# Kernel optimization log

Measured on AMD Instinct MI355X. Metric: run time of the kernel, lower is better.

## Reference

```python
import jax, jax.numpy as jnp
import numpy as np

B, T, D = 4, 4096, 768      # batch, tokens, n_embd
S = 1024                    # memory_slots (divides T -> adaptive pool == window mean)
K = 8                       # memory_topk
RW = 0.1                    # memory_retrieval_weight


def setup_inputs() -> dict:
    key = jax.random.key(0)
    ks = jax.random.split(key, 10)
    w = 1.0 / np.sqrt(D).astype(np.float32)
    return {
        "x": jax.random.normal(ks[0], (B, T, D), jnp.float32),
        "Wq": jax.random.normal(ks[1], (D, D), jnp.float32) * w,
        "bq": jnp.zeros((D,), jnp.float32),
        "Wk": jax.random.normal(ks[2], (D, D), jnp.float32) * w,
        "bk": jnp.zeros((D,), jnp.float32),
        "Wv": jax.random.normal(ks[3], (D, D), jnp.float32) * w,
        "bv": jnp.zeros((D,), jnp.float32),
        "Wp": jax.random.normal(ks[4], (D, D), jnp.float32) * w,
        "bp": jnp.zeros((D,), jnp.float32),
        "persistent_memory": jax.random.normal(ks[5], (S, D), jnp.float32),
    }


def reference(x, Wq, bq, Wk, bk, Wv, bv, Wp, bp, persistent_memory):
    # _build_memory_slots: adaptive_avg_pool1d to S slots; T % S == 0 so it is a window mean
    pooled = x.reshape(B, S, T // S, D).mean(axis=2)                    # [B,S,D]
    pers = jnp.broadcast_to(persistent_memory[None], (B, S, D))         # persistent bank
    slots = jnp.concatenate([pooled, pers], axis=1)                     # [B,2S,D]

    q = x @ Wq + bq                                                     # [B,T,D]
    k = slots @ Wk + bk                                                 # [B,2S,D]
    v = slots @ Wv + bv                                                 # [B,2S,D]

    scores = jnp.einsum('btd,bsd->bts', q, k) / jnp.sqrt(jnp.float32(D))  # [B,T,2S]
    top_s, top_i = jax.lax.top_k(scores, K)                             # [B,T,K]
    w = jax.nn.softmax(top_s, axis=-1)                                  # softmax over top-k only

    # gather top-k values: [B,T,K,D]
    vg = jnp.take_along_axis(v, top_i.reshape(B, T * K)[:, :, None], axis=1)
    vg = vg.reshape(B, T, K, D)
    retrieved = jnp.einsum('btk,btkd->btd', w, vg)                      # weighted combine

    return RW * (retrieved @ Wp + bp)                                   # proj * retrieval_weight
```

## Files before the change

kernel.cpp:

```cpp
#include <hip/hip_runtime.h>
#include <math.h>

#define BB 4
#define TT 4096
#define DD 768
#define SS 1024
#define S2 2048
#define KTOP 8
#define RWEIGHT 0.1f
#define TAU 2e-4f
#define AMB_CAP 64

typedef __attribute__((ext_vector_type(8))) _Float16 f16x8;
typedef __attribute__((ext_vector_type(4))) float f32x4;
typedef _Float16 f16;

__global__ __launch_bounds__(256) void build_pooled_all(
    const float* __restrict__ x, float* __restrict__ slots)
{
    int i = blockIdx.x * 256 + threadIdx.x;
    int s2 = i / DD;
    int d = i - s2 * DD;
    int b = s2 >> 10, s = s2 & 1023;
    const float* xb = x + (size_t)b * TT * DD + (size_t)(4 * s) * DD + d;
    slots[i] = 0.25f * (xb[0] + xb[DD] + xb[2 * DD] + xb[3 * DD]);
}

__global__ __launch_bounds__(256) void transpose_all(
    const float* __restrict__ W0, const float* __restrict__ W1,
    const float* __restrict__ W2, const float* __restrict__ W3,
    float* __restrict__ T0, float* __restrict__ T1,
    float* __restrict__ T2, float* __restrict__ T3)
{
    const float* W = (blockIdx.z == 0) ? W0 : (blockIdx.z == 1) ? W1
                   : (blockIdx.z == 2) ? W2 : W3;
    float* WT = (blockIdx.z == 0) ? T0 : (blockIdx.z == 1) ? T1
              : (blockIdx.z == 2) ? T2 : T3;
    __shared__ float t[32][33];
    int bx = blockIdx.x * 32, by = blockIdx.y * 32;
    int lx = threadIdx.x & 31, ly = threadIdx.x >> 5;
#pragma unroll
    for (int r = 0; r < 32; r += 8)
        t[ly + r][lx] = W[(size_t)(bx + ly + r) * 768 + by + lx];
    __syncthreads();
#pragma unroll
    for (int r = 0; r < 32; r += 8)
        WT[(size_t)(by + ly + r) * 768 + bx + lx] = t[lx][ly + r];
}

__global__ void zeroN(int* p) { p[threadIdx.x] = 0; }

__global__ __launch_bounds__(256) void producers(
    const float* __restrict__ xq, const float* __restrict__ aslots,
    const f16* __restrict__ aproj,
    const float* __restrict__ WqT, const float* __restrict__ WkT,
    const float* __restrict__ WvT, const float* __restrict__ WpT,
    const float* __restrict__ bq, const float* __restrict__ bk,
    const float* __restrict__ bv, const float* __restrict__ bp,
    f16* __restrict__ qh, f16* __restrict__ qm,
    f16* __restrict__ kh, f16* __restrict__ km,
    f16* __restrict__ v16, float* __restrict__ oproj,
    int n_q, int n_kv, int rowoff)
{
    __shared__ f16 LAh[4096], LAm[4096], LBh[4096], LBm[4096];
    const int tid = threadIdx.x;
    const int lane = tid & 63;
    const int wc = (tid >> 6) & 1;
    const int wr = (tid >> 7) & 1;

    int t = blockIdx.x, mode, bx, by;
    if (t < n_q) { mode = 0; bx = t % 6; by = t / 6; }
    else if (t < n_q + n_kv) { mode = 1; int u = t - n_q; bx = u % 6; by = u / 6; }
    else if (t < n_q + 2 * n_kv) { mode = 2; int u = t - n_q - n_kv; bx = u % 6; by = u / 6; }
    else { mode = 3; int u = t - n_q - 2 * n_kv; bx = u % 6; by = u / 6; }

    const int srow = tid >> 1, c0 = tid & 1;
    const int p0 = c0 ^ (srow & 3) ^ ((srow >> 2) & 1);
    const int wo0 = srow * 32 + p0 * 8, wo1 = wo0 ^ 16;
    const int csw = (((lane >> 4) ^ (lane & 3) ^ ((lane >> 2) & 1)) * 8);
    const int arow0 = by * 128;
    const size_t bn = (size_t)bx * 128;

    f32x4 acc[4][4];
#pragma unroll
    for (int i = 0; i < 4; ++i)
#pragma unroll
        for (int j = 0; j < 4; ++j) acc[i][j] = (f32x4){0.f, 0.f, 0.f, 0.f};

    const int orow0 = wr * 64 + (lane >> 4) * 4;
    const int ocol0 = wc * 64 + (lane & 15);

    if (mode <= 1) {
        const float* A  = (mode == 0) ? xq : aslots;
        const float* BT = (mode == 0) ? WqT : WkT;
        const float* bi = (mode == 0) ? bq : bk;
        f16* Ch = (mode == 0) ? qh : kh;
        f16* Cm = (mode == 0) ? qm : km;
        const int crow0 = ((mode == 0) ? 0 : rowoff) + arow0;
        const float* pa = A + (size_t)(arow0 + srow) * 768 + c0 * 8;
        const float* pb = BT + (bn + srow) * 768 + c0 * 8;

        for (int k0 = 0; k0 < 768; k0 += 32) {
            float4 a0 = *(const float4*)(pa + k0);
            float4 a1 = *(const float4*)(pa + k0 + 4);
            float4 a2 = *(const float4*)(pa + k0 + 16);
            float4 a3 = *(const float4*)(pa + k0 + 20);
            float4 b0 = *(const float4*)(pb + k0);
            float4 b1 = *(const float4*)(pb + k0 + 4);
            float4 b2 = *(const float4*)(pb + k0 + 16);
            float4 b3 = *(const float4*)(pb + k0 + 20);
            __syncthreads();
            {
                float av[16] = {a0.x, a0.y, a0.z, a0.w, a1.x, a1.y, a1.z, a1.w,
                                a2.x, a2.y, a2.z, a2.w, a3.x, a3.y, a3.z, a3.w};
                float bv2[16] = {b0.x, b0.y, b0.z, b0.w, b1.x, b1.y, b1.z, b1.w,
                                 b2.x, b2.y, b2.z, b2.w, b3.x, b3.y, b3.z, b3.w};
                f16x8 h, m;
#pragma unroll
                for (int j = 0; j < 8; ++j) {
                    f16 hh = (f16)av[j]; h[j] = hh; m[j] = (f16)(av[j] - (float)hh);
                }
                *(f16x8*)&LAh[wo0] = h; *(f16x8*)&LAm[wo0] = m;
#pragma unroll
                for (int j = 0; j < 8; ++j) {
                    f16 hh = (f16)av[j + 8]; h[j] = hh; m[j] = (f16)(av[j + 8] - (float)hh);
                }
                *(f16x8*)&LAh[wo1] = h; *(f16x8*)&LAm[wo1] = m;
#pragma unroll
                for (int j = 0; j < 8; ++j) {
                    f16 hh = (f16)bv2[j]; h[j] = hh; m[j] = (f16)(bv2[j] - (float)hh);
                }
                *(f16x8*)&LBh[wo0] = h; *(f16x8*)&LBm[wo0] = m;
#pragma unroll
                for (int j = 0; j < 8; ++j) {
                    f16 hh = (f16)bv2[j + 8]; h[j] = hh; m[j] = (f16)(bv2[j + 8] - (float)hh);
                }
                *(f16x8*)&LBh[wo1] = h; *(f16x8*)&LBm[wo1] = m;
            }
            __syncthreads();

            f16x8 fah[4], fam[4], fbh[4], fbm[4];
#pragma unroll
            for (int mi = 0; mi < 4; ++mi) {
                int off = (wr * 64 + mi * 16 + (lane & 15)) * 32 + csw;
                fah[mi] = *(const f16x8*)&LAh[off];
                fam[mi] = *(const f16x8*)&LAm[off];
            }
#pragma unroll
            for (int ni = 0; ni < 4; ++ni) {
                int off = (wc * 64 + ni * 16 + (lane & 15)) * 32 + csw;
                fbh[ni] = *(const f16x8*)&LBh[off];
                fbm[ni] = *(const f16x8*)&LBm[off];
            }
#pragma unroll
            for (int mi = 0; mi < 4; ++mi)
#pragma unroll
                for (int ni = 0; ni < 4; ++ni) {
                    acc[mi][ni] = __builtin_amdgcn_mfma_f32_16x16x32_f16(
                        fah[mi], fbh[ni], acc[mi][ni], 0, 0, 0);
                    acc[mi][ni] = __builtin_amdgcn_mfma_f32_16x16x32_f16(
                        fah[mi], fbm[ni], acc[mi][ni], 0, 0, 0);
                    acc[mi][ni] = __builtin_amdgcn_mfma_f32_16x16x32_f16(
                        fam[mi], fbh[ni], acc[mi][ni], 0, 0, 0);
                }
        }
#pragma unroll
        for (int mi = 0; mi < 4; ++mi)
#pragma unroll
            for (int ni = 0; ni < 4; ++ni) {
                size_t col = bn + ocol0 + ni * 16;
                float badd = bi[col];
                size_t rbase = (size_t)crow0 + orow0 + mi * 16;
#pragma unroll
                for (int r = 0; r < 4; ++r) {
                    float val = acc[mi][ni][r] + badd;
                    f16 h = (f16)val;
                    size_t idx = (rbase + r) * 768 + col;
                    Ch[idx] = h;
                    Cm[idx] = (f16)(val - (float)h);
                }
            }
    } else if (mode == 2) {
        const int crow0 = rowoff + arow0;
        const float* pa = aslots + (size_t)(arow0 + srow) * 768 + c0 * 8;
        const float* pb = WvT + (bn + srow) * 768 + c0 * 8;
        for (int k0 = 0; k0 < 768; k0 += 32) {
            float4 a0 = *(const float4*)(pa + k0);
            float4 a1 = *(const float4*)(pa + k0 + 4);
            float4 a2 = *(const float4*)(pa + k0 + 16);
            float4 a3 = *(const float4*)(pa + k0 + 20);
            float4 b0 = *(const float4*)(pb + k0);
            float4 b1 = *(const float4*)(pb + k0 + 4);
            float4 b2 = *(const float4*)(pb + k0 + 16);
            float4 b3 = *(const float4*)(pb + k0 + 20);
            __syncthreads();
            {
                f16x8 h;
                h[0] = (f16)a0.x; h[1] = (f16)a0.y; h[2] = (f16)a0.z; h[3] = (f16)a0.w;
                h[4] = (f16)a1.x; h[5] = (f16)a1.y; h[6] = (f16)a1.z; h[7] = (f16)a1.w;
                *(f16x8*)&LAh[wo0] = h;
                h[0] = (f16)a2.x; h[1] = (f16)a2.y; h[2] = (f16)a2.z; h[3] = (f16)a2.w;
                h[4] = (f16)a3.x; h[5] = (f16)a3.y; h[6] = (f16)a3.z; h[7] = (f16)a3.w;
                *(f16x8*)&LAh[wo1] = h;
                h[0] = (f16)b0.x; h[1] = (f16)b0.y; h[2] = (f16)b0.z; h[3] = (f16)b0.w;
                h[4] = (f16)b1.x; h[5] = (f16)b1.y; h[6] = (f16)b1.z; h[7] = (f16)b1.w;
                *(f16x8*)&LBh[wo0] = h;
                h[0] = (f16)b2.x; h[1] = (f16)b2.y; h[2] = (f16)b2.z; h[3] = (f16)b2.w;
                h[4] = (f16)b3.x; h[5] = (f16)b3.y; h[6] = (f16)b3.z; h[7] = (f16)b3.w;
                *(f16x8*)&LBh[wo1] = h;
            }
            __syncthreads();
            f16x8 fah[4], fbh[4];
#pragma unroll
            for (int mi = 0; mi < 4; ++mi)
                fah[mi] = *(const f16x8*)&LAh[(wr * 64 + mi * 16 + (lane & 15)) * 32 + csw];
#pragma unroll
            for (int ni = 0; ni < 4; ++ni)
                fbh[ni] = *(const f16x8*)&LBh[(wc * 64 + ni * 16 + (lane & 15)) * 32 + csw];
#pragma unroll
            for (int mi = 0; mi < 4; ++mi)
#pragma unroll
                for (int ni = 0; ni < 4; ++ni)
                    acc[mi][ni] = __builtin_amdgcn_mfma_f32_16x16x32_f16(
                        fah[mi], fbh[ni], acc[mi][ni], 0, 0, 0);
        }
#pragma unroll
        for (int mi = 0; mi < 4; ++mi)
#pragma unroll
            for (int ni = 0; ni < 4; ++ni) {
                size_t col = bn + ocol0 + ni * 16;
                float badd = bv[col];
                size_t rbase = (size_t)crow0 + orow0 + mi * 16;
#pragma unroll
                for (int r = 0; r < 4; ++r)
                    v16[(rbase + r) * 768 + col] = (f16)(acc[mi][ni][r] + badd);
            }
    } else {
        const f16* pa = aproj + (size_t)(arow0 + srow) * 768 + c0 * 8;
        const float* pb = WpT + (bn + srow) * 768 + c0 * 8;
        for (int k0 = 0; k0 < 768; k0 += 32) {
            f16x8 ah0 = *(const f16x8*)(pa + k0);
            f16x8 ah1 = *(const f16x8*)(pa + k0 + 16);
            float4 b0 = *(const float4*)(pb + k0);
            float4 b1 = *(const float4*)(pb + k0 + 4);
            float4 b2 = *(const float4*)(pb + k0 + 16);
            float4 b3 = *(const float4*)(pb + k0 + 20);
            __syncthreads();
            *(f16x8*)&LAh[wo0] = ah0;
            *(f16x8*)&LAh[wo1] = ah1;
            {
                f16x8 h;
                h[0] = (f16)b0.x; h[1] = (f16)b0.y; h[2] = (f16)b0.z; h[3] = (f16)b0.w;
                h[4] = (f16)b1.x; h[5] = (f16)b1.y; h[6] = (f16)b1.z; h[7] = (f16)b1.w;
                *(f16x8*)&LBh[wo0] = h;
                h[0] = (f16)b2.x; h[1] = (f16)b2.y; h[2] = (f16)b2.z; h[3] = (f16)b2.w;
                h[4] = (f16)b3.x; h[5] = (f16)b3.y; h[6] = (f16)b3.z; h[7] = (f16)b3.w;
                *(f16x8*)&LBh[wo1] = h;
            }
            __syncthreads();
            f16x8 fah[4], fbh[4];
#pragma unroll
            for (int mi = 0; mi < 4; ++mi)
                fah[mi] = *(const f16x8*)&LAh[(wr * 64 + mi * 16 + (lane & 15)) * 32 + csw];
#pragma unroll
            for (int ni = 0; ni < 4; ++ni)
                fbh[ni] = *(const f16x8*)&LBh[(wc * 64 + ni * 16 + (lane & 15)) * 32 + csw];
#pragma unroll
            for (int mi = 0; mi < 4; ++mi)
#pragma unroll
                for (int ni = 0; ni < 4; ++ni)
                    acc[mi][ni] = __builtin_amdgcn_mfma_f32_16x16x32_f16(
                        fah[mi], fbh[ni], acc[mi][ni], 0, 0, 0);
        }
#pragma unroll
        for (int mi = 0; mi < 4; ++mi)
#pragma unroll
            for (int ni = 0; ni < 4; ++ni) {
                size_t col = bn + ocol0 + ni * 16;
                float badd = RWEIGHT * bp[col];
                size_t rbase = (size_t)arow0 + orow0 + mi * 16;
#pragma unroll
                for (int r = 0; r < 4; ++r)
                    oproj[(rbase + r) * 768 + col] = RWEIGHT * acc[mi][ni][r] + badd;
            }
    }
}

__global__ __launch_bounds__(256) void scores_planes(
    const f16* __restrict__ qh, const f16* __restrict__ qm,
    const f16* __restrict__ kh, const f16* __restrict__ km,
    float* __restrict__ C, float alpha)
{
    __shared__ f16 LAh[4096], LAm[4096], LBh[4096], LBm[4096];
    const int tid = threadIdx.x;
    const int lane = tid & 63;
    const int wc = (tid >> 6) & 1;
    const int wr = (tid >> 7) & 1;
    const size_t bm = (size_t)blockIdx.y * 128;
    const size_t bn = (size_t)blockIdx.x * 128;

    f32x4 acc[4][4];
#pragma unroll
    for (int i = 0; i < 4; ++i)
#pragma unroll
        for (int j = 0; j < 4; ++j) acc[i][j] = (f32x4){0.f, 0.f, 0.f, 0.f};

    const int srow = tid >> 1, c0 = tid & 1;
    const int p0 = c0 ^ (srow & 3) ^ ((srow >> 2) & 1);
    const int wo0 = srow * 32 + p0 * 8, wo1 = wo0 ^ 16;
    const int csw = (((lane >> 4) ^ (lane & 3) ^ ((lane >> 2) & 1)) * 8);

    const f16* pah = qh + (bm + srow) * 768 + c0 * 8;
    const f16* pam = qm + (bm + srow) * 768 + c0 * 8;
    const f16* pbh = kh + (bn + srow) * 768 + c0 * 8;
    const f16* pbm = km + (bn + srow) * 768 + c0 * 8;

    for (int k0 = 0; k0 < 768; k0 += 32) {
        f16x8 ah0 = *(const f16x8*)(pah + k0);
        f16x8 ah1 = *(const f16x8*)(pah + k0 + 16);
        f16x8 am0 = *(const f16x8*)(pam + k0);
        f16x8 am1 = *(const f16x8*)(pam + k0 + 16);
        f16x8 bh0 = *(const f16x8*)(pbh + k0);
        f16x8 bh1 = *(const f16x8*)(pbh + k0 + 16);
        f16x8 bm0 = *(const f16x8*)(pbm + k0);
        f16x8 bm1 = *(const f16x8*)(pbm + k0 + 16);
        __syncthreads();
        *(f16x8*)&LAh[wo0] = ah0; *(f16x8*)&LAh[wo1] = ah1;
        *(f16x8*)&LAm[wo0] = am0; *(f16x8*)&LAm[wo1] = am1;
        *(f16x8*)&LBh[wo0] = bh0; *(f16x8*)&LBh[wo1] = bh1;
        *(f16x8*)&LBm[wo0] = bm0; *(f16x8*)&LBm[wo1] = bm1;
        __syncthreads();

        f16x8 fah[4], fam[4], fbh[4], fbm[4];
#pragma unroll
        for (int mi = 0; mi < 4; ++mi) {
            int off = (wr * 64 + mi * 16 + (lane & 15)) * 32 + csw;
            fah[mi] = *(const f16x8*)&LAh[off];
            fam[mi] = *(const f16x8*)&LAm[off];
        }
#pragma unroll
        for (int ni = 0; ni < 4; ++ni) {
            int off = (wc * 64 + ni * 16 + (lane & 15)) * 32 + csw;
            fbh[ni] = *(const f16x8*)&LBh[off];
            fbm[ni] = *(const f16x8*)&LBm[off];
        }
#pragma unroll
        for (int mi = 0; mi < 4; ++mi)
#pragma unroll
            for (int ni = 0; ni < 4; ++ni) {
                acc[mi][ni] = __builtin_amdgcn_mfma_f32_16x16x32_f16(
                    fah[mi], fbh[ni], acc[mi][ni], 0, 0, 0);
                acc[mi][ni] = __builtin_amdgcn_mfma_f32_16x16x32_f16(
                    fah[mi], fbm[ni], acc[mi][ni], 0, 0, 0);
                acc[mi][ni] = __builtin_amdgcn_mfma_f32_16x16x32_f16(
                    fam[mi], fbh[ni], acc[mi][ni], 0, 0, 0);
            }
    }

    const int orow0 = wr * 64 + (lane >> 4) * 4;
    const int ocol0 = wc * 64 + (lane & 15);
#pragma unroll
    for (int mi = 0; mi < 4; ++mi)
#pragma unroll
        for (int ni = 0; ni < 4; ++ni) {
            size_t col = bn + ocol0 + ni * 16;
            size_t rbase = bm + orow0 + mi * 16;
#pragma unroll
            for (int r = 0; r < 4; ++r)
                C[(rbase + r) * S2 + col] = alpha * acc[mi][ni][r];
        }
}

template <int NR>
__device__ void wave_topk(const float* __restrict__ srow, int lane,
                          float* topv, int* topi)
{
    float vals[32];
#pragma unroll
    for (int i = 0; i < 32; ++i) vals[i] = srow[lane + (i << 6)];
#pragma unroll
    for (int r = 0; r < NR; ++r) {
        float bvv = -3.4e38f; int bii = 0x7fffffff;
#pragma unroll
        for (int i = 0; i < 32; ++i)
            if (vals[i] > bvv) { bvv = vals[i]; bii = lane + (i << 6); }
#pragma unroll
        for (int off = 32; off > 0; off >>= 1) {
            float ov = __shfl_xor(bvv, off);
            int   oi = __shfl_xor(bii, off);
            if (ov > bvv || (ov == bvv && oi < bii)) { bvv = ov; bii = oi; }
        }
        topv[r] = bvv; topi[r] = bii;
        if ((bii & 63) == lane) vals[bii >> 6] = -3.4e38f;
    }
}

__global__ __launch_bounds__(256) void select_combine(
    const float* __restrict__ scores, const f16* __restrict__ v16,
    f16* __restrict__ retrc,
    int* __restrict__ amb_count, int* __restrict__ amb_rows,
    int* __restrict__ cand)
{
    const int lane = threadIdx.x & 63;
    const int wave = threadIdx.x >> 6;
    const int row = blockIdx.x * 4 + wave;

    const float* srow = scores + (size_t)row * S2;
    float vals[32];
#pragma unroll
    for (int i = 0; i < 32; ++i) vals[i] = srow[lane + (i << 6)];

    float topv[16]; int topi[16];
    bool amb = false;
    int nr = 9;
    for (int r = 0; r < 16; ++r) {
        if (r >= nr) break;
        float bvv = -3.4e38f; int bii = 0x7fffffff;
#pragma unroll
        for (int i = 0; i < 32; ++i)
            if (vals[i] > bvv) { bvv = vals[i]; bii = lane + (i << 6); }
#pragma unroll
        for (int off = 32; off > 0; off >>= 1) {
            float ov = __shfl_xor(bvv, off);
            int   oi = __shfl_xor(bii, off);
            if (ov > bvv || (ov == bvv && oi < bii)) { bvv = ov; bii = oi; }
        }
        topv[r] = bvv; topi[r] = bii;
        if ((bii & 63) == lane) vals[bii >> 6] = -3.4e38f;
        if (r == 8) {
            amb = (topv[7] - topv[8]) < TAU;
            if (amb) nr = 16;
        }
    }

    if (amb) {
        int idx = 0;
        if (lane == 0) idx = atomicAdd(amb_count, 1);
        idx = __shfl(idx, 0);
        if (idx < AMB_CAP) {
            if (lane == 0) amb_rows[idx] = row;
            if (lane < 16) cand[idx * 16 + lane] = topi[lane];
        }
    }

    float m = topv[0], w[KTOP], sum = 0.f;
#pragma unroll
    for (int r = 0; r < KTOP; ++r) { w[r] = expf(topv[r] - m); sum += w[r]; }
    float inv = 1.f / sum;
#pragma unroll
    for (int r = 0; r < KTOP; ++r) w[r] *= inv;

    for (int c = lane; c < 96; c += 64) {
        float o[8] = {0, 0, 0, 0, 0, 0, 0, 0};
#pragma unroll
        for (int r = 0; r < KTOP; ++r) {
            f16x8 vv = *(const f16x8*)&v16[(size_t)topi[r] * 768 + c * 8];
#pragma unroll
            for (int j = 0; j < 8; ++j) o[j] += w[r] * (float)vv[j];
        }
        f16x8 hx;
#pragma unroll
        for (int j = 0; j < 8; ++j) hx[j] = (f16)o[j];
        *(f16x8*)&retrc[(size_t)row * 768 + c * 8] = hx;
    }
}

__global__ __launch_bounds__(256) void fixup_q(
    const int* __restrict__ amb_count, const int* __restrict__ amb_rows,
    const float* __restrict__ xc, const float* __restrict__ Wq,
    const float* __restrict__ bq, double* __restrict__ q64buf)
{
    int n = *amb_count; if (n > AMB_CAP) n = AMB_CAP;
    const int i = blockIdx.y;
    if (i >= n) return;
    const int tid = threadIdx.x;
    const int jl = tid & 63;
    const int ks = tid >> 6;
    const int j = blockIdx.x * 64 + jl;
    const int row = amb_rows[i];

    __shared__ float xs[768];
    __shared__ double ps[4][64];
    for (int t = tid; t < 768; t += 256) xs[t] = xc[(size_t)row * 768 + t];
    __syncthreads();

    double a0 = 0.0, a1 = 0.0;
    const float* wp = Wq + j;
    const int k0 = ks * 192;
#pragma unroll 8
    for (int k = 0; k < 192; k += 2) {
        a0 = fma((double)xs[k0 + k],     (double)wp[(size_t)(k0 + k) * 768],     a0);
        a1 = fma((double)xs[k0 + k + 1], (double)wp[(size_t)(k0 + k + 1) * 768], a1);
    }
    ps[ks][jl] = a0 + a1;
    __syncthreads();
    if (ks == 0)
        q64buf[(size_t)i * 768 + j] =
            ((ps[0][jl] + ps[1][jl]) + (ps[2][jl] + ps[3][jl])) + (double)bq[j];
}

__global__ __launch_bounds__(256) void fixup_u(
    const int* __restrict__ amb_count,
    const float* __restrict__ WkT, const float* __restrict__ bk,
    const double* __restrict__ q64buf,
    double* __restrict__ ubuf, double* __restrict__ bkqbuf)
{
    int n = *amb_count; if (n > AMB_CAP) n = AMB_CAP;
    const int i = blockIdx.y;
    if (i >= n) return;
    const int tid = threadIdx.x;
    const int tl = tid & 63;
    const int js = tid >> 6;
    const int t = blockIdx.x * 64 + tl;

    __shared__ double qs[768];
    __shared__ double ps[4][64];
    const double* qrow = q64buf + (size_t)i * 768;
    for (int k = tid; k < 768; k += 256) qs[k] = qrow[k];
    __syncthreads();

    double a0 = 0.0, a1 = 0.0;
    const float* wp = WkT + t;
    const int j0 = js * 192;
#pragma unroll 8
    for (int k = 0; k < 192; k += 2) {
        a0 = fma((double)wp[(size_t)(j0 + k) * 768],     qs[j0 + k],     a0);
        a1 = fma((double)wp[(size_t)(j0 + k + 1) * 768], qs[j0 + k + 1], a1);
    }
    ps[js][tl] = a0 + a1;
    __syncthreads();
    if (js == 0)
        ubuf[(size_t)i * 768 + t] = (ps[0][tl] + ps[1][tl]) + (ps[2][tl] + ps[3][tl]);

    if (blockIdx.x == 0 && tid < 64) {
        double p = 0.0;
#pragma unroll
        for (int c = 0; c < 12; ++c) {
            int jj = tid + (c << 6);
            p = fma((double)bk[jj], qs[jj], p);
        }
#pragma unroll
        for (int off = 32; off; off >>= 1) p += __shfl_xor(p, off);
        if (tid == 0) bkqbuf[i] = p;
    }
}

__global__ __launch_bounds__(256) void fixup_sel(
    const int* __restrict__ amb_count, const int* __restrict__ amb_rows,
    const float* __restrict__ xb, const float* __restrict__ pm,
    const int* __restrict__ cand, const double* __restrict__ ubuf,
    const double* __restrict__ bkqbuf, const f16* __restrict__ v16,
    f16* __restrict__ retrc)
{
    int n = *amb_count; if (n > AMB_CAP) n = AMB_CAP;
    const int i = blockIdx.x;
    if (i >= n) return;
    const int tid = threadIdx.x;
    const int lane = tid & 63;
    const int wave = tid >> 6;
    const int row = amb_rows[i];

    __shared__ double us[768];
    __shared__ double cs_s[16];
    __shared__ float wsm[KTOP];
    __shared__ int seli[KTOP];

    const double* urow = ubuf + (size_t)i * 768;
    for (int t = tid; t < 768; t += 256) us[t] = urow[t];
    __syncthreads();

    const double ISQ = 1.0 / sqrt((double)DD);
    const double bkq = bkqbuf[i];
#pragma unroll
    for (int c = wave; c < 16; c += 4) {
        int s = cand[i * 16 + c];
        double p = 0.0;
        if (s < SS) {
            const float* xr = xb + (size_t)(4 * s) * 768;
#pragma unroll
            for (int t = 0; t < 12; ++t) {
                int j2 = lane + (t << 6);
                double sv = 0.25 * ((double)xr[j2] + (double)xr[j2 + 768] +
                                    (double)xr[j2 + 1536] + (double)xr[j2 + 2304]);
                p = fma(sv, us[j2], p);
            }
        } else {
            const float* pr = pm + (size_t)(s - SS) * 768;
#pragma unroll
            for (int t = 0; t < 12; ++t) {
                int j2 = lane + (t << 6);
                p = fma((double)pr[j2], us[j2], p);
            }
        }
#pragma unroll
        for (int off = 32; off; off >>= 1) p += __shfl_xor(p, off);
        if (lane == 0) cs_s[c] = (p + bkq) * ISQ;
    }
    __syncthreads();

    if (tid == 0) {
        double cs[16]; int ci[16];
        for (int c = 0; c < 16; ++c) { cs[c] = cs_s[c]; ci[c] = cand[i * 16 + c]; }
        unsigned used = 0;
        double sv[KTOP]; int sx[KTOP];
        for (int r = 0; r < KTOP; ++r) {
            int bi = -1;
            for (int c = 0; c < 16; ++c) {
                if (used & (1u << c)) continue;
                if (bi < 0 || cs[c] > cs[bi] ||
                    (cs[c] == cs[bi] && ci[c] < ci[bi])) bi = c;
            }
            used |= (1u << bi); sv[r] = cs[bi]; sx[r] = ci[bi];
        }
        double mx = sv[0], es[KTOP], ssum = 0.0;
        for (int r = 0; r < KTOP; ++r) { es[r] = exp(sv[r] - mx); ssum += es[r]; }
        for (int r = 0; r < KTOP; ++r) { wsm[r] = (float)(es[r] / ssum); seli[r] = sx[r]; }
    }
    __syncthreads();
    for (int c = tid; c < 96; c += 256) {
        float o[8] = {0, 0, 0, 0, 0, 0, 0, 0};
#pragma unroll
        for (int r = 0; r < KTOP; ++r) {
            f16x8 vv = *(const f16x8*)&v16[(size_t)seli[r] * 768 + c * 8];
#pragma unroll
            for (int j = 0; j < 8; ++j) o[j] += wsm[r] * (float)vv[j];
        }
        f16x8 hx;
#pragma unroll
        for (int j = 0; j < 8; ++j) hx[j] = (f16)o[j];
        *(f16x8*)&retrc[(size_t)row * 768 + c * 8] = hx;
    }
}

extern "C" void kernel_launch(void* const* d_in, const int* in_sizes, int n_in,
                              void* d_out, int out_size, void* d_ws, size_t ws_size,
                              hipStream_t stream)
{
    const float* x  = (const float*)d_in[0];
    const float* Wq = (const float*)d_in[1];
    const float* bq = (const float*)d_in[2];
    const float* Wk = (const float*)d_in[3];
    const float* bk = (const float*)d_in[4];
    const float* Wv = (const float*)d_in[5];
    const float* bv = (const float*)d_in[6];
    const float* Wp = (const float*)d_in[7];
    const float* bp = (const float*)d_in[8];
    const float* pm = (const float*)d_in[9];
    float* out = (float*)d_out;
    float* ws  = (float*)d_ws;

    const float inv_sqrt_d = (float)(1.0 / sqrt((double)DD));
    const size_t TD  = (size_t)TT * DD;
    const size_t SD  = (size_t)SS * DD;
    const size_t WSZ = (size_t)DD * DD;

    float* p = ws;
    float* WqT = p; p += WSZ;
    float* WkT = p; p += WSZ;
    float* WvT = p; p += WSZ;
    float* WpT = p; p += WSZ;
    float* slots_all = p; p += (size_t)BB * SD;
    f16* qh = (f16*)p; p += TD / 2;
    f16* qm = (f16*)p; p += TD / 2;
    f16* kh = (f16*)p; p += SD;
    f16* km = (f16*)p; p += SD;
    f16* v16 = (f16*)p; p += SD;
    f16* retrA = (f16*)p; p += TD / 2;
    f16* retrB = (f16*)p; p += TD / 2;
    double* q64buf = (double*)p; p += (size_t)AMB_CAP * DD * 2;
    double* ubuf   = (double*)p; p += (size_t)AMB_CAP * DD * 2;
    double* bkqbuf = (double*)p; p += AMB_CAP * 2;
    int* cand = (int*)p; p += (size_t)AMB_CAP * 16;
    int* ambc = (int*)p; p += 64;
    int* ambrows = (int*)p; p += AMB_CAP;
    float* scores = p;
    size_t used = (size_t)(p - ws);

    long tc = TT;
    while (tc > 512 && (used + (size_t)tc * S2) * 4 > ws_size) tc >>= 1;

    transpose_all<<<dim3(24, 24, 4), 256, 0, stream>>>(
        Wq, Wk, Wv, Wp, WqT, WkT, WvT, WpT);
    zeroN<<<1, 64, 0, stream>>>(ambc);
    build_pooled_all<<<(BB * SS * DD) / 256, 256, 0, stream>>>(x, slots_all);

    producers<<<96, 256, 0, stream>>>(
        nullptr, pm, nullptr, WqT, WkT, WvT, WpT, bq, bk, bv, bp,
        qh, qm, kh, km, v16, nullptr, 0, 48, SS);

    int cidx = 0;
    for (int b = 0; b < BB; ++b) {
        const float* xb = x + (size_t)b * TD;
        const float* slots_b = slots_all + (size_t)b * SD;
        f16* rcur = (b & 1) ? retrB : retrA;
        f16* rprev = (b & 1) ? retrA : retrB;
        int np = b ? 192 : 0;

        producers<<<288 + np, 256, 0, stream>>>(
            xb, slots_b, rprev, WqT, WkT, WvT, WpT, bq, bk, bv, bp,
            qh, qm, kh, km, v16, out + (size_t)(b - 1) * TD, 192, 48, 0);

        for (long t0 = 0; t0 < TT; t0 += tc) {
            int* cc = ambc + cidx; cidx = (cidx + 1) & 63;
            scores_planes<<<dim3(16, tc / 128), 256, 0, stream>>>(
                qh + (size_t)t0 * DD, qm + (size_t)t0 * DD, kh, km,
                scores, inv_sqrt_d);
            select_combine<<<tc / 4, 256, 0, stream>>>(
                scores, v16, rcur + (size_t)t0 * DD, cc, ambrows, cand);
            fixup_q<<<dim3(12, AMB_CAP), 256, 0, stream>>>(
                cc, ambrows, xb + (size_t)t0 * DD, Wq, bq, q64buf);
            fixup_u<<<dim3(12, AMB_CAP), 256, 0, stream>>>(
                cc, WkT, bk, q64buf, ubuf, bkqbuf);
            fixup_sel<<<AMB_CAP, 256, 0, stream>>>(
                cc, ambrows, xb, pm, cand, ubuf, bkqbuf, v16,
                rcur + (size_t)t0 * DD);
        }
    }

    f16* rlast = ((BB - 1) & 1) ? retrB : retrA;
    producers<<<192, 256, 0, stream>>>(
        nullptr, nullptr, rlast, WqT, WkT, WvT, WpT, bq, bk, bv, bp,
        qh, qm, kh, km, v16, out + (size_t)(BB - 1) * TD, 0, 0, 0);
}
```

Measured before the change: 706.1 us.

## Defer ambiguous-row top-k fixups to one batched pass after projection

Instead of running three fixup kernels after every score chunk, select_combine now records global row ids, the old softmax weights, and copies of the 16 candidate value rows. After the final projection, four kernels recompute the exact selection once for all ambiguous rows. A new fixD applies the weight change through Wp as a delta added to the output. This removes many small per-chunk launches and serialisation points, at the cost of extra saving work in select_combine and a doubled ambiguity cap.

```diff
diff --git a/kernel.cpp b/kernel.cpp
--- a/kernel.cpp
+++ b/kernel.cpp
@@ -9,7 +9,7 @@
 #define KTOP 8
 #define RWEIGHT 0.1f
 #define TAU 2e-4f
-#define AMB_CAP 64
+#define AMB_CAP 128
 
 typedef __attribute__((ext_vector_type(8))) _Float16 f16x8;
 typedef __attribute__((ext_vector_type(4))) float f32x4;
@@ -371,35 +371,11 @@
         }
 }
 
-template <int NR>
-__device__ void wave_topk(const float* __restrict__ srow, int lane,
-                          float* topv, int* topi)
-{
-    float vals[32];
-#pragma unroll
-    for (int i = 0; i < 32; ++i) vals[i] = srow[lane + (i << 6)];
-#pragma unroll
-    for (int r = 0; r < NR; ++r) {
-        float bvv = -3.4e38f; int bii = 0x7fffffff;
-#pragma unroll
-        for (int i = 0; i < 32; ++i)
-            if (vals[i] > bvv) { bvv = vals[i]; bii = lane + (i << 6); }
-#pragma unroll
-        for (int off = 32; off > 0; off >>= 1) {
-            float ov = __shfl_xor(bvv, off);
-            int   oi = __shfl_xor(bii, off);
-            if (ov > bvv || (ov == bvv && oi < bii)) { bvv = ov; bii = oi; }
-        }
-        topv[r] = bvv; topi[r] = bii;
-        if ((bii & 63) == lane) vals[bii >> 6] = -3.4e38f;
-    }
-}
-
 __global__ __launch_bounds__(256) void select_combine(
     const float* __restrict__ scores, const f16* __restrict__ v16,
-    f16* __restrict__ retrc,
-    int* __restrict__ amb_count, int* __restrict__ amb_rows,
-    int* __restrict__ cand)
+    f16* __restrict__ retrc, int gbase,
+    int* __restrict__ amb_count, int* __restrict__ amb_grow,
+    int* __restrict__ cand, float* __restrict__ oldw, f16* __restrict__ vsave)
 {
     const int lane = threadIdx.x & 63;
     const int wave = threadIdx.x >> 6;
@@ -433,22 +409,29 @@
         }
     }
 
+    float m = topv[0], w[KTOP], sum = 0.f;
+#pragma unroll
+    for (int r = 0; r < KTOP; ++r) { w[r] = expf(topv[r] - m); sum += w[r]; }
+    float inv = 1.f / sum;
+#pragma unroll
+    for (int r = 0; r < KTOP; ++r) w[r] *= inv;
+
     if (amb) {
         int idx = 0;
         if (lane == 0) idx = atomicAdd(amb_count, 1);
         idx = __shfl(idx, 0);
         if (idx < AMB_CAP) {
-            if (lane == 0) amb_rows[idx] = row;
+            if (lane == 0) amb_grow[idx] = gbase + row;
             if (lane < 16) cand[idx * 16 + lane] = topi[lane];
-        }
-    }
-
-    float m = topv[0], w[KTOP], sum = 0.f;
-#pragma unroll
-    for (int r = 0; r < KTOP; ++r) { w[r] = expf(topv[r] - m); sum += w[r]; }
-    float inv = 1.f / sum;
-#pragma unroll
-    for (int r = 0; r < KTOP; ++r) w[r] *= inv;
+            if (lane < KTOP) oldw[idx * KTOP + lane] = w[lane];
+            f16* vs = vsave + (size_t)idx * 16 * 768;
+            for (int cc = lane; cc < 16 * 96; cc += 64) {
+                int cr = cc / 96, ch = cc - cr * 96;
+                *(f16x8*)&vs[(size_t)cr * 768 + ch * 8] =
+                    *(const f16x8*)&v16[(size_t)topi[cr] * 768 + ch * 8];
+            }
+        }
+    }
 
     for (int c = lane; c < 96; c += 64) {
         float o[8] = {0, 0, 0, 0, 0, 0, 0, 0};
@@ -465,9 +448,9 @@
     }
 }
 
-__global__ __launch_bounds__(256) void fixup_q(
-    const int* __restrict__ amb_count, const int* __restrict__ amb_rows,
-    const float* __restrict__ xc, const float* __restrict__ Wq,
+__global__ __launch_bounds__(256) void fixA(
+    const int* __restrict__ amb_count, const int* __restrict__ amb_grow,
+    const float* __restrict__ x, const float* __restrict__ Wq,
     const float* __restrict__ bq, double* __restrict__ q64buf)
 {
     int n = *amb_count; if (n > AMB_CAP) n = AMB_CAP;
@@ -477,11 +460,11 @@
     const int jl = tid & 63;
     const int ks = tid >> 6;
     const int j = blockIdx.x * 64 + jl;
-    const int row = amb_rows[i];
+    const int grow = amb_grow[i];
 
     __shared__ float xs[768];
     __shared__ double ps[4][64];
-    for (int t = tid; t < 768; t += 256) xs[t] = xc[(size_t)row * 768 + t];
+    for (int t = tid; t < 768; t += 256) xs[t] = x[(size_t)grow * 768 + t];
     __syncthreads();
 
     double a0 = 0.0, a1 = 0.0;
@@ -499,7 +482,7 @@
             ((ps[0][jl] + ps[1][jl]) + (ps[2][jl] + ps[3][jl])) + (double)bq[j];
 }
 
-__global__ __launch_bounds__(256) void fixup_u(
+__global__ __launch_bounds__(256) void fixB(
     const int* __restrict__ amb_count,
     const float* __restrict__ WkT, const float* __restrict__ bk,
     const double* __restrict__ q64buf,
@@ -545,12 +528,12 @@
     }
 }
 
-__global__ __launch_bounds__(256) void fixup_sel(
-    const int* __restrict__ amb_count, const int* __restrict__ amb_rows,
-    const float* __restrict__ xb, const float* __restrict__ pm,
-    const int* __restrict__ cand, const double* __restrict__ ubuf,
-    const double* __restrict__ bkqbuf, const f16* __restrict__ v16,
-    f16* __restrict__ retrc)
+__global__ __launch_bounds__(256) void fixC(
+    const int* __restrict__ amb_count, const int* __restrict__ amb_grow,
+    const float* __restrict__ x, const float* __restrict__ pm,
+    const int* __restrict__ cand, const float* __restrict__ oldw,
+    const double* __restrict__ ubuf, const double* __restrict__ bkqbuf,
+    const f16* __restrict__ vsave, float* __restrict__ dret)
 {
     int n = *amb_count; if (n > AMB_CAP) n = AMB_CAP;
     const int i = blockIdx.x;
@@ -558,12 +541,12 @@
     const int tid = threadIdx.x;
     const int lane = tid & 63;
     const int wave = tid >> 6;
-    const int row = amb_rows[i];
+    const int grow = amb_grow[i];
+    const float* xb = x + (size_t)(grow >> 12) * TT * 768;
 
     __shared__ double us[768];
     __shared__ double cs_s[16];
-    __shared__ float wsm[KTOP];
-    __shared__ int seli[KTOP];
+    __shared__ float coef[16];
 
     const double* urow = ubuf + (size_t)i * 768;
     for (int t = tid; t < 768; t += 256) us[t] = urow[t];
@@ -602,7 +585,7 @@
         double cs[16]; int ci[16];
         for (int c = 0; c < 16; ++c) { cs[c] = cs_s[c]; ci[c] = cand[i * 16 + c]; }
         unsigned used = 0;
-        double sv[KTOP]; int sx[KTOP];
+        double sv[KTOP]; int sp[KTOP];
         for (int r = 0; r < KTOP; ++r) {
             int bi = -1;
             for (int c = 0; c < 16; ++c) {
@@ -610,26 +593,56 @@
                 if (bi < 0 || cs[c] > cs[bi] ||
                     (cs[c] == cs[bi] && ci[c] < ci[bi])) bi = c;
             }
-            used |= (1u << bi); sv[r] = cs[bi]; sx[r] = ci[bi];
+            used |= (1u << bi); sv[r] = cs[bi]; sp[r] = bi;
         }
         double mx = sv[0], es[KTOP], ssum = 0.0;
         for (int r = 0; r < KTOP; ++r) { es[r] = exp(sv[r] - mx); ssum += es[r]; }
-        for (int r = 0; r < KTOP; ++r) { wsm[r] = (float)(es[r] / ssum); seli[r] = sx[r]; }
-    }
-    __syncthreads();
-    for (int c = tid; c < 96; c += 256) {
-        float o[8] = {0, 0, 0, 0, 0, 0, 0, 0};
-#pragma unroll
-        for (int r = 0; r < KTOP; ++r) {
-            f16x8 vv = *(const f16x8*)&v16[(size_t)seli[r] * 768 + c * 8];
-#pragma unroll
-            for (int j = 0; j < 8; ++j) o[j] += wsm[r] * (float)vv[j];
-        }
-        f16x8 hx;
-#pragma unroll
-        for (int j = 0; j < 8; ++j) hx[j] = (f16)o[j];
-        *(f16x8*)&retrc[(size_t)row * 768 + c * 8] = hx;
-    }
+        for (int c = 0; c < 16; ++c) coef[c] = (c < KTOP) ? -oldw[i * KTOP + c] : 0.f;
+        for (int r = 0; r < KTOP; ++r) coef[sp[r]] += (float)(es[r] / ssum);
+    }
+    __syncthreads();
+
+    const f16* vs = vsave + (size_t)i * 16 * 768;
+    for (int j = tid; j < 768; j += 256) {
+        float d = 0.f;
+#pragma unroll
+        for (int c = 0; c < 16; ++c) d += coef[c] * (float)vs[(size_t)c * 768 + j];
+        dret[(size_t)i * 768 + j] = d;
+    }
+}
+
+__global__ __launch_bounds__(256) void fixD(
+    const int* __restrict__ amb_count, const int* __restrict__ amb_grow,
+    const float* __restrict__ dret, const float* __restrict__ Wp,
+    float* __restrict__ out)
+{
+    int n = *amb_count; if (n > AMB_CAP) n = AMB_CAP;
+    const int i = blockIdx.y;
+    if (i >= n) return;
+    const int tid = threadIdx.x;
+    const int jl = tid & 63;
+    const int ks = tid >> 6;
+    const int j = blockIdx.x * 64 + jl;
+    const int grow = amb_grow[i];
+
+    __shared__ float ds[768];
+    __shared__ float ps[4][64];
+    for (int t = tid; t < 768; t += 256) ds[t] = dret[(size_t)i * 768 + t];
+    __syncthreads();
+
+    float a0 = 0.f, a1 = 0.f;
+    const float* wp = Wp + j;
+    const int k0 = ks * 192;
+#pragma unroll 8
+    for (int k = 0; k < 192; k += 2) {
+        a0 = fmaf(ds[k0 + k],     wp[(size_t)(k0 + k) * 768],     a0);
+        a1 = fmaf(ds[k0 + k + 1], wp[(size_t)(k0 + k + 1) * 768], a1);
+    }
+    ps[ks][jl] = a0 + a1;
+    __syncthreads();
+    if (ks == 0)
+        out[(size_t)grow * 768 + j] +=
+            RWEIGHT * ((ps[0][jl] + ps[1][jl]) + (ps[2][jl] + ps[3][jl]));
 }
 
 extern "C" void kernel_launch(void* const* d_in, const int* in_sizes, int n_in,
@@ -671,8 +684,11 @@
     double* ubuf   = (double*)p; p += (size_t)AMB_CAP * DD * 2;
     double* bkqbuf = (double*)p; p += AMB_CAP * 2;
     int* cand = (int*)p; p += (size_t)AMB_CAP * 16;
+    float* oldw = p; p += (size_t)AMB_CAP * KTOP;
+    f16* vsave = (f16*)p; p += (size_t)AMB_CAP * 16 * DD / 2;
+    float* dret = p; p += (size_t)AMB_CAP * DD;
     int* ambc = (int*)p; p += 64;
-    int* ambrows = (int*)p; p += AMB_CAP;
+    int* ambgrow = (int*)p; p += AMB_CAP;
     float* scores = p;
     size_t used = (size_t)(p - ws);
 
@@ -688,7 +704,6 @@
         nullptr, pm, nullptr, WqT, WkT, WvT, WpT, bq, bk, bv, bp,
         qh, qm, kh, km, v16, nullptr, 0, 48, SS);
 
-    int cidx = 0;
     for (int b = 0; b < BB; ++b) {
         const float* xb = x + (size_t)b * TD;
         const float* slots_b = slots_all + (size_t)b * SD;
@@ -701,19 +716,12 @@
             qh, qm, kh, km, v16, out + (size_t)(b - 1) * TD, 192, 48, 0);
 
         for (long t0 = 0; t0 < TT; t0 += tc) {
-            int* cc = ambc + cidx; cidx = (cidx + 1) & 63;
             scores_planes<<<dim3(16, tc / 128), 256, 0, stream>>>(
                 qh + (size_t)t0 * DD, qm + (size_t)t0 * DD, kh, km,
                 scores, inv_sqrt_d);
             select_combine<<<tc / 4, 256, 0, stream>>>(
-                scores, v16, rcur + (size_t)t0 * DD, cc, ambrows, cand);
-            fixup_q<<<dim3(12, AMB_CAP), 256, 0, stream>>>(
-                cc, ambrows, xb + (size_t)t0 * DD, Wq, bq, q64buf);
-            fixup_u<<<dim3(12, AMB_CAP), 256, 0, stream>>>(
-                cc, WkT, bk, q64buf, ubuf, bkqbuf);
-            fixup_sel<<<AMB_CAP, 256, 0, stream>>>(
-                cc, ambrows, xb, pm, cand, ubuf, bkqbuf, v16,
-                rcur + (size_t)t0 * DD);
+                scores, v16, rcur + (size_t)t0 * DD, b * TT + (int)t0,
+                ambc, ambgrow, cand, oldw, vsave);
         }
     }
 
@@ -721,4 +729,10 @@
     producers<<<192, 256, 0, stream>>>(
         nullptr, nullptr, rlast, WqT, WkT, WvT, WpT, bq, bk, bv, bp,
         qh, qm, kh, km, v16, out + (size_t)(BB - 1) * TD, 0, 0, 0);
-}
+
+    fixA<<<dim3(12, AMB_CAP), 256, 0, stream>>>(ambc, ambgrow, x, Wq, bq, q64buf);
+    fixB<<<dim3(12, AMB_CAP), 256, 0, stream>>>(ambc, WkT, bk, q64buf, ubuf, bkqbuf);
+    fixC<<<AMB_CAP, 256, 0, stream>>>(ambc, ambgrow, x, pm, cand, oldw,
+                                      ubuf, bkqbuf, vsave, dret);
+    fixD<<<dim3(12, AMB_CAP), 256, 0, stream>>>(ambc, ambgrow, dret, Wp, out);
+}
```

After: 648.5 us. -8.2%, faster.
